# Optimization experiments

Measured on AMD Instinct MI355X. Metric: run time of the kernel, lower is better.

Reference implementation:

```python
import jax, jax.numpy as jnp
import numpy as np

EMBED = 1024
HEADS = 16
HEAD_DIM = EMBED // HEADS


def setup_inputs() -> dict:
    key = jax.random.key(0)
    ks = jax.random.split(key, 11)
    B, S, E = 4, 2048, EMBED
    scale = 1.0 / np.sqrt(E)
    inp = {
        "Q": jax.random.normal(ks[0], (B, S, E), jnp.float32),
        "K": jax.random.normal(ks[1], (B, S, E), jnp.float32),
        "V": jax.random.normal(ks[2], (B, S, E), jnp.float32),
        "Wq": jax.random.normal(ks[3], (E, E), jnp.float32) * scale,
        "Wk": jax.random.normal(ks[4], (E, E), jnp.float32) * scale,
        "Wv": jax.random.normal(ks[5], (E, E), jnp.float32) * scale,
        "Wo": jax.random.normal(ks[6], (E, E), jnp.float32) * scale,
        "bq": jax.random.normal(ks[7], (E,), jnp.float32) * 0.01,
        "bk": jax.random.normal(ks[8], (E,), jnp.float32) * 0.01,
        "bv": jax.random.normal(ks[9], (E,), jnp.float32) * 0.01,
        "bo": jax.random.normal(ks[10], (E,), jnp.float32) * 0.01,
    }
    return inp


def reference(Q, K, V, Wq, Wk, Wv, Wo, bq, bk, bv, bo):
    B, S, E = Q.shape
    H, Dh = HEADS, HEAD_DIM
    # linear projections (torch Linear: x @ W.T + b)
    q = (Q @ Wq.T + bq).reshape(B, S, H, Dh).transpose(0, 2, 1, 3)  # [B,H,S,Dh]
    k = (K @ Wk.T + bk).reshape(B, S, H, Dh).transpose(0, 2, 1, 3)
    v = (V @ Wv.T + bv).reshape(B, S, H, Dh).transpose(0, 2, 1, 3)
    # scores [B,H,S,S]
    A = jnp.einsum('bhqd,bhkd->bhqk', q, k) / np.sqrt(Dh).astype(np.float32)
    # causal mask (mask=True)
    causal = jnp.tril(jnp.ones((S, S), dtype=bool))
    A = jnp.where(causal, A, -jnp.inf)
    w = jax.nn.softmax(A, axis=-1)
    out = jnp.einsum('bhqk,bhkd->bhqd', w, v)  # [B,H,S,Dh]
    out = out.transpose(0, 2, 1, 3).reshape(B, S, E)
    return out @ Wo.T + bo
```

## Files before the change

### kernel.cpp

```cpp
#include <hip/hip_runtime.h>
#include <hip/hip_bf16.h>
#include <hip/hip_fp16.h>

#define E_DIM 1024
#define N_HEADS 16
#define DH 64
#define BATCH 4
#define SEQ 2048
#define MROWS (BATCH * SEQ)
#define NQT 16

using half8 = __attribute__((ext_vector_type(8))) _Float16;
using half4v = __attribute__((ext_vector_type(4))) _Float16;
using fp16x2 = __attribute__((ext_vector_type(2))) __fp16;
using f32x4 = __attribute__((ext_vector_type(4))) float;

#define LOG2E 1.44269504088896340736f

__device__ inline half8 ld8(const _Float16* p) { return *(const half8*)p; }

__device__ inline uint32_t lds_off(const void* p) {
    return (uint32_t)(uintptr_t)(const __attribute__((address_space(3))) char*)p;
}

__device__ inline float exp2fast(float x) {
    float r;
    asm("v_exp_f32 %0, %1" : "=v"(r) : "v"(x));
    return r;
}

__global__ void cast3_f16(const float* __restrict__ a0, const float* __restrict__ a1,
                          const float* __restrict__ a2,
                          _Float16* __restrict__ o0, _Float16* __restrict__ o1,
                          _Float16* __restrict__ o2, int n4) {
    const int z = blockIdx.y;
    const float* in = z == 0 ? a0 : z == 1 ? a1 : a2;
    _Float16* out = z == 0 ? o0 : z == 1 ? o1 : o2;
    int i = blockIdx.x * blockDim.x + threadIdx.x;
    if (i < n4) {
        float4 v = *(const float4*)(in + (size_t)i * 4);
        half4v o;
        o[0] = (_Float16)v.x; o[1] = (_Float16)v.y;
        o[2] = (_Float16)v.z; o[3] = (_Float16)v.w;
        *(half4v*)(out + (size_t)i * 4) = o;
    }
}
__global__ void cast4_f16(const float* __restrict__ a0, const float* __restrict__ a1,
                          const float* __restrict__ a2, const float* __restrict__ a3,
                          _Float16* __restrict__ o0, _Float16* __restrict__ o1,
                          _Float16* __restrict__ o2, _Float16* __restrict__ o3, int n4) {
    const int z = blockIdx.y;
    const float* in = z == 0 ? a0 : z == 1 ? a1 : z == 2 ? a2 : a3;
    _Float16* out = z == 0 ? o0 : z == 1 ? o1 : z == 2 ? o2 : o3;
    int i = blockIdx.x * blockDim.x + threadIdx.x;
    if (i < n4) {
        float4 v = *(const float4*)(in + (size_t)i * 4);
        half4v o;
        o[0] = (_Float16)v.x; o[1] = (_Float16)v.y;
        o[2] = (_Float16)v.z; o[3] = (_Float16)v.w;
        *(half4v*)(out + (size_t)i * 4) = o;
    }
}

template <int MODE>
__device__ __forceinline__ void gemm_body(
    const _Float16* __restrict__ A, const _Float16* __restrict__ Bt,
    const float* __restrict__ bias, void* __restrict__ outp,
    int N, int K, float scale, _Float16* As, _Float16* Bs)
{
    const int t = threadIdx.x;
    const int w = t >> 6, l = t & 63;
    const int wr = w >> 1, wc = w & 1;
    const int lr = l & 15, lg = l >> 4;
    const long row0 = (long)blockIdx.x * 128;
    const long col0 = (long)blockIdx.y * 128;
    f32x4 acc[4][4] = {};

    for (int k0 = 0; k0 < K; k0 += 32) {
        __syncthreads();
        #pragma unroll
        for (int p = 0; p < 2; ++p) {
            const int n = p * 256 + t;
            const int row = n >> 2, c8 = (n & 3) << 3;
            const _Float16* ga = &A[(size_t)(row0 + row) * K + k0 + c8];
            const _Float16* gb = &Bt[(size_t)(col0 + row) * K + k0 + c8];
            __builtin_amdgcn_global_load_lds(
                (const __attribute__((address_space(1))) unsigned int*)ga,
                (__attribute__((address_space(3))) unsigned int*)((char*)As + n * 16), 16, 0, 0);
            __builtin_amdgcn_global_load_lds(
                (const __attribute__((address_space(1))) unsigned int*)gb,
                (__attribute__((address_space(3))) unsigned int*)((char*)Bs + n * 16), 16, 0, 0);
        }
        __syncthreads();
        half8 af[4], bf[4];
        #pragma unroll
        for (int i = 0; i < 4; i++) {
            af[i] = *(const half8*)&As[(wr * 64 + i * 16 + lr) * 32 + lg * 8];
            bf[i] = *(const half8*)&Bs[(wc * 64 + i * 16 + lr) * 32 + lg * 8];
        }
        #pragma unroll
        for (int i = 0; i < 4; i++)
            #pragma unroll
            for (int j = 0; j < 4; j++)
                acc[i][j] = __builtin_amdgcn_mfma_f32_16x16x32_f16(af[i], bf[j], acc[i][j], 0, 0, 0);
    }

    #pragma unroll
    for (int i = 0; i < 4; i++)
        #pragma unroll
        for (int j = 0; j < 4; j++)
            #pragma unroll
            for (int r = 0; r < 4; r++) {
                long row = row0 + wr * 64 + i * 16 + lg * 4 + r;
                long col = col0 + wc * 64 + j * 16 + lr;
                float v = acc[i][j][r] + bias[col];
                if (MODE == 0) {
                    ((float*)outp)[row * N + col] = v;
                } else {
                    long b = row >> 11, s = row & 2047;
                    long h = col >> 6, d = col & 63;
                    ((_Float16*)outp)[(((b * N_HEADS + h) * SEQ + s) << 6) + d] =
                        (_Float16)(v * scale);
                }
            }
}

__global__ __launch_bounds__(256) void gemm_qkv(
    const _Float16* __restrict__ A0, const _Float16* __restrict__ A1,
    const _Float16* __restrict__ A2,
    const _Float16* __restrict__ W0, const _Float16* __restrict__ W1,
    const _Float16* __restrict__ W2,
    const float* __restrict__ b0, const float* __restrict__ b1,
    const float* __restrict__ b2,
    _Float16* __restrict__ o0, _Float16* __restrict__ o1, _Float16* __restrict__ o2)
{
    __shared__ _Float16 As[128 * 32];
    __shared__ _Float16 Bs[128 * 32];
    const int z = blockIdx.z;
    const _Float16* A = z == 0 ? A0 : z == 1 ? A1 : A2;
    const _Float16* W = z == 0 ? W0 : z == 1 ? W1 : W2;
    const float* bia = z == 0 ? b0 : z == 1 ? b1 : b2;
    _Float16* o = z == 0 ? o0 : z == 1 ? o1 : o2;
    const float scale = z == 0 ? (0.125f * LOG2E) : 1.0f;
    gemm_body<1>(A, W, bia, o, E_DIM, E_DIM, scale, As, Bs);
}

__global__ __launch_bounds__(256) void gemm_out(
    const _Float16* __restrict__ A, const _Float16* __restrict__ W,
    const float* __restrict__ bias, float* __restrict__ o)
{
    __shared__ _Float16 As[128 * 32];
    __shared__ _Float16 Bs[128 * 32];
    gemm_body<0>(A, W, bias, o, E_DIM, E_DIM, 1.0f, As, Bs);
}

__global__ __launch_bounds__(256) void attn_fwd(
    const _Float16* __restrict__ qb, const _Float16* __restrict__ kb,
    const _Float16* __restrict__ vb, _Float16* __restrict__ ob)
{
    __shared__ _Float16 sK[2 * 4096];
    __shared__ _Float16 sV[2 * 4096];
    const int bh = blockIdx.x;
    const int p = blockIdx.y;
    const int t = threadIdx.x;
    const int w = t >> 6, l = t & 63;
    const int lr = l & 15, lg = l >> 4;
    const _Float16* qh = qb + (size_t)bh * SEQ * DH;
    const _Float16* kh = kb + (size_t)bh * SEQ * DH;
    const _Float16* vh = vb + (size_t)bh * SEQ * DH;

    const int srow = t >> 3, sc16 = t & 7;
    const uint32_t kd0 = (uint32_t)((srow * 128 + sc16 * 16) ^ ((srow & 7) << 4));
    const uint32_t kd1 = (uint32_t)(((srow + 32) * 128 + sc16 * 16) ^ ((srow & 7) << 4));
    const uint32_t vd0 = (uint32_t)(((srow >> 2) * 256 + (sc16 >> 1) * 64 + (srow & 3) * 16 + (sc16 & 1) * 8) * 2);
    const uint32_t vd1 = (uint32_t)((((srow + 32) >> 2) * 256 + (sc16 >> 1) * 64 + (srow & 3) * 16 + (sc16 & 1) * 8) * 2);
    char* sKc = (char*)sK;
    char* sVc = (char*)sV;
    const uint32_t vldsbase = lds_off(sV);
    const int b = bh >> 4, h = bh & 15;

    #pragma unroll 1
    for (int seg = 0; seg < 2; ++seg) {
        const int tile = seg == 0 ? p : (NQT - 1 - p);
        const int nt = 2 * tile + 2;
        const int q0 = tile * 128 + w * 16;
        const int q1 = q0 + 64;

        half8 qf00 = ld8(&qh[(q0 + lr) * DH + lg * 8]);
        half8 qf01 = ld8(&qh[(q0 + lr) * DH + 32 + lg * 8]);
        half8 qf10 = ld8(&qh[(q1 + lr) * DH + lg * 8]);
        half8 qf11 = ld8(&qh[(q1 + lr) * DH + 32 + lg * 8]);

        f32x4 acc0[4] = {}, acc1[4] = {};
        float m0 = -1e30f, l0 = 0.f, m1 = -1e30f, l1 = 0.f;

        __syncthreads();
        {
            const _Float16* kp = &kh[srow * DH + sc16 * 8];
            const _Float16* vp = &vh[srow * DH + sc16 * 8];
            half8 a = ld8(kp), bb = ld8(kp + 32 * DH);
            half8 c = ld8(vp), d = ld8(vp + 32 * DH);
            *(half8*)(sKc + kd0) = a;
            *(half8*)(sKc + kd1) = bb;
            *(half8*)(sVc + vd0) = c;
            *(half8*)(sVc + vd1) = d;
        }
        __syncthreads();

        int cur = 0;
        for (int it = 0; it < nt; ++it) {
            half8 nk0, nk1, nv0, nv1;
            const bool more = (it + 1 < nt);
            if (more) {
                const _Float16* kp = &kh[((it + 1) * 64 + srow) * DH + sc16 * 8];
                const _Float16* vp = &vh[((it + 1) * 64 + srow) * DH + sc16 * 8];
                nk0 = ld8(kp); nk1 = ld8(kp + 32 * DH);
                nv0 = ld8(vp); nv1 = ld8(vp + 32 * DH);
            }

            const char* kbuf = sKc + (cur ? 8192 : 0);
            const uint32_t vbuf = vldsbase + (cur ? 8192u : 0u);
            const bool a0 = (it <= 2 * tile);
            const bool diag0 = (it == 2 * tile);
            const bool diag1 = (it == 2 * tile + 1);

            f32x4 st0[4], st1[4];
            __builtin_amdgcn_s_setprio(1);
            #pragma unroll
            for (int sub = 0; sub < 4; ++sub) {
                const int row = sub * 16 + lr;
                half8 kf0 = *(const half8*)(kbuf + ((row * 128 + lg * 16) ^ ((row & 7) << 4)));
                half8 kf1 = *(const half8*)(kbuf + ((row * 128 + 64 + lg * 16) ^ ((row & 7) << 4)));
                f32x4 s1 = {};
                s1 = __builtin_amdgcn_mfma_f32_16x16x32_f16(kf0, qf10, s1, 0, 0, 0);
                s1 = __builtin_amdgcn_mfma_f32_16x16x32_f16(kf1, qf11, s1, 0, 0, 0);
                st1[sub] = s1;
                if (a0) {
                    f32x4 s0 = {};
                    s0 = __builtin_amdgcn_mfma_f32_16x16x32_f16(kf0, qf00, s0, 0, 0, 0);
                    s0 = __builtin_amdgcn_mfma_f32_16x16x32_f16(kf1, qf01, s0, 0, 0, 0);
                    st0[sub] = s0;
                }
            }
            __builtin_amdgcn_s_setprio(0);

            half4v pa0[4], pa1[4];
            bool skip0 = true;
            if (a0) {
                if (diag0) {
                    #pragma unroll
                    for (int sub = 0; sub < 4; ++sub)
                        #pragma unroll
                        for (int r = 0; r < 4; ++r)
                            if (sub * 16 + lg * 4 + r > w * 16 + lr) st0[sub][r] = -1e30f;
                }
                float tmax = -1e30f;
                #pragma unroll
                for (int sub = 0; sub < 4; ++sub)
                    #pragma unroll
                    for (int r = 0; r < 4; ++r) tmax = fmaxf(tmax, st0[sub][r]);
                tmax = fmaxf(tmax, __shfl_xor(tmax, 16, 64));
                tmax = fmaxf(tmax, __shfl_xor(tmax, 32, 64));
                skip0 = __all(tmax <= m0 + 10.0f);
                float fscale = 1.0f;
                if (!skip0) {
                    const float m_new = fmaxf(m0, tmax);
                    fscale = exp2fast(m0 - m_new);
                    m0 = m_new;
                }
                float psum = 0.f;
                #pragma unroll
                for (int sub = 0; sub < 4; ++sub) {
                    float pv[4];
                    #pragma unroll
                    for (int r = 0; r < 4; ++r) { pv[r] = exp2fast(st0[sub][r] - m0); psum += pv[r]; }
                    fp16x2 lo = __builtin_amdgcn_cvt_pkrtz(pv[0], pv[1]);
                    fp16x2 hi = __builtin_amdgcn_cvt_pkrtz(pv[2], pv[3]);
                    pa0[sub][0] = (_Float16)lo[0]; pa0[sub][1] = (_Float16)lo[1];
                    pa0[sub][2] = (_Float16)hi[0]; pa0[sub][3] = (_Float16)hi[1];
                }
                l0 = l0 * fscale + psum;
                if (!skip0) {
                    #pragma unroll
                    for (int r = 0; r < 4; ++r) {
                        const float fr = __shfl(fscale, lg * 4 + r, 64);
                        acc0[0][r] *= fr; acc0[1][r] *= fr; acc0[2][r] *= fr; acc0[3][r] *= fr;
                    }
                }
            }

            {
                if (diag1) {
                    #pragma unroll
                    for (int sub = 0; sub < 4; ++sub)
                        #pragma unroll
                        for (int r = 0; r < 4; ++r)
                            if (sub * 16 + lg * 4 + r > w * 16 + lr) st1[sub][r] = -1e30f;
                }
                float tmax = -1e30f;
                #pragma unroll
                for (int sub = 0; sub < 4; ++sub)
                    #pragma unroll
                    for (int r = 0; r < 4; ++r) tmax = fmaxf(tmax, st1[sub][r]);
                tmax = fmaxf(tmax, __shfl_xor(tmax, 16, 64));
                tmax = fmaxf(tmax, __shfl_xor(tmax, 32, 64));
                const bool skip = __all(tmax <= m1 + 10.0f);
                float fscale = 1.0f;
                if (!skip) {
                    const float m_new = fmaxf(m1, tmax);
                    fscale = exp2fast(m1 - m_new);
                    m1 = m_new;
                }
                float psum = 0.f;
                #pragma unroll
                for (int sub = 0; sub < 4; ++sub) {
                    float pv[4];
                    #pragma unroll
                    for (int r = 0; r < 4; ++r) { pv[r] = exp2fast(st1[sub][r] - m1); psum += pv[r]; }
                    fp16x2 lo = __builtin_amdgcn_cvt_pkrtz(pv[0], pv[1]);
                    fp16x2 hi = __builtin_amdgcn_cvt_pkrtz(pv[2], pv[3]);
                    pa1[sub][0] = (_Float16)lo[0]; pa1[sub][1] = (_Float16)lo[1];
                    pa1[sub][2] = (_Float16)hi[0]; pa1[sub][3] = (_Float16)hi[1];
                }
                l1 = l1 * fscale + psum;
                if (!skip) {
                    #pragma unroll
                    for (int r = 0; r < 4; ++r) {
                        const float fr = __shfl(fscale, lg * 4 + r, 64);
                        acc1[0][r] *= fr; acc1[1][r] *= fr; acc1[2][r] *= fr; acc1[3][r] *= fr;
                    }
                }
            }

            __builtin_amdgcn_s_setprio(1);
            #pragma unroll
            for (int sub = 0; sub < 4; ++sub) {
                const uint32_t a0addr = vbuf + (uint32_t)((sub * 4 + lg) * 512 + lr * 8);
                half4v vf0, vf1, vf2, vf3;
                asm volatile("ds_read_b64_tr_b16 %0, %1" : "=v"(vf0) : "v"(a0addr));
                asm volatile("ds_read_b64_tr_b16 %0, %1 offset:128" : "=v"(vf1) : "v"(a0addr));
                asm volatile("ds_read_b64_tr_b16 %0, %1 offset:256" : "=v"(vf2) : "v"(a0addr));
                asm volatile("ds_read_b64_tr_b16 %0, %1 offset:384" : "=v"(vf3) : "v"(a0addr));
                asm volatile("s_waitcnt lgkmcnt(0)");
                __builtin_amdgcn_sched_barrier(0);
                acc1[0] = __builtin_amdgcn_mfma_f32_16x16x16f16(pa1[sub], vf0, acc1[0], 0, 0, 0);
                acc1[1] = __builtin_amdgcn_mfma_f32_16x16x16f16(pa1[sub], vf1, acc1[1], 0, 0, 0);
                acc1[2] = __builtin_amdgcn_mfma_f32_16x16x16f16(pa1[sub], vf2, acc1[2], 0, 0, 0);
                acc1[3] = __builtin_amdgcn_mfma_f32_16x16x16f16(pa1[sub], vf3, acc1[3], 0, 0, 0);
                if (a0) {
                    acc0[0] = __builtin_amdgcn_mfma_f32_16x16x16f16(pa0[sub], vf0, acc0[0], 0, 0, 0);
                    acc0[1] = __builtin_amdgcn_mfma_f32_16x16x16f16(pa0[sub], vf1, acc0[1], 0, 0, 0);
                    acc0[2] = __builtin_amdgcn_mfma_f32_16x16x16f16(pa0[sub], vf2, acc0[2], 0, 0, 0);
                    acc0[3] = __builtin_amdgcn_mfma_f32_16x16x16f16(pa0[sub], vf3, acc0[3], 0, 0, 0);
                }
            }
            __builtin_amdgcn_s_setprio(0);

            if (more) {
                char* kd = sKc + (cur ? 0 : 8192);
                char* vd = sVc + (cur ? 0 : 8192);
                *(half8*)(kd + kd0) = nk0;
                *(half8*)(kd + kd1) = nk1;
                *(half8*)(vd + vd0) = nv0;
                *(half8*)(vd + vd1) = nv1;
            }
            __syncthreads();
            cur ^= 1;
        }

        l0 += __shfl_xor(l0, 16, 64); l0 += __shfl_xor(l0, 32, 64);
        l1 += __shfl_xor(l1, 16, 64); l1 += __shfl_xor(l1, 32, 64);
        const float inv0 = 1.f / l0, inv1 = 1.f / l1;
        #pragma unroll
        for (int r = 0; r < 4; ++r) {
            const float ir0 = __shfl(inv0, lg * 4 + r, 64);
            const float ir1 = __shfl(inv1, lg * 4 + r, 64);
            const int qr0 = q0 + lg * 4 + r;
            const int qr1 = q1 + lg * 4 + r;
            #pragma unroll
            for (int db = 0; db < 4; ++db) {
                ob[((size_t)(b * SEQ + qr0)) * E_DIM + h * DH + db * 16 + lr] =
                    (_Float16)(acc0[db][r] * ir0);
                ob[((size_t)(b * SEQ + qr1)) * E_DIM + h * DH + db * 16 + lr] =
                    (_Float16)(acc1[db][r] * ir1);
            }
        }
    }
}

extern "C" void kernel_launch(void* const* d_in, const int* in_sizes, int n_in,
                              void* d_out, int out_size, void* d_ws, size_t ws_size,
                              hipStream_t stream) {
    const float* Q  = (const float*)d_in[0];
    const float* K  = (const float*)d_in[1];
    const float* V  = (const float*)d_in[2];
    const float* Wq = (const float*)d_in[3];
    const float* Wk = (const float*)d_in[4];
    const float* Wv = (const float*)d_in[5];
    const float* Wo = (const float*)d_in[6];
    const float* bq = (const float*)d_in[7];
    const float* bk = (const float*)d_in[8];
    const float* bv = (const float*)d_in[9];
    const float* bo = (const float*)d_in[10];

    const size_t NX = (size_t)MROWS * E_DIM;
    const size_t NW = (size_t)E_DIM * E_DIM;

    _Float16* ws  = (_Float16*)d_ws;
    _Float16* Xq  = ws;
    _Float16* Xk  = Xq + NX;
    _Float16* Xv  = Xk + NX;
    _Float16* hWq = Xv + NX;
    _Float16* hWk = hWq + NW;
    _Float16* hWv = hWk + NW;
    _Float16* hWo = hWv + NW;
    _Float16* qbf = hWo + NW;
    _Float16* kbf = qbf + NX;
    _Float16* vbf = kbf + NX;
    _Float16* aof = vbf + NX;

    const int n4x = (int)(NX / 4), n4w = (int)(NW / 4);
    cast3_f16<<<dim3((n4x + 255) / 256, 3), 256, 0, stream>>>(Q, K, V, Xq, Xk, Xv, n4x);
    cast4_f16<<<dim3((n4w + 255) / 256, 4), 256, 0, stream>>>(Wq, Wk, Wv, Wo, hWq, hWk, hWv, hWo, n4w);

    dim3 gg3(MROWS / 128, E_DIM / 128, 3);
    gemm_qkv<<<gg3, 256, 0, stream>>>(Xq, Xk, Xv, hWq, hWk, hWv, bq, bk, bv, qbf, kbf, vbf);

    attn_fwd<<<dim3(BATCH * N_HEADS, NQT / 2), 256, 0, stream>>>(qbf, kbf, vbf, aof);

    dim3 gg(MROWS / 128, E_DIM / 128);
    gemm_out<<<gg, 256, 0, stream>>>(aof, hWo, bo, (float*)d_out);
}
```

Before: 219.1 us.

## Stream K/V tiles into triple-buffered LDS via direct global-to-LDS loads

Replaces the register-staged double-buffered K/V loads in the attention kernel with direct global_load_lds transfers into a three-slot LDS ring, prefetching two tiles ahead with vmcnt waits and one barrier per iteration. The swizzle moves from the LDS write address to the global read address, so the existing read layout is kept. The change also uses a tree-shaped max reduction and fdot2-based row sums on the packed fp16 probabilities. It uses more LDS (48KB), which may lower occupancy, and the row sums are now taken from the fp16-rounded values.

```diff
diff --git a/kernel.cpp b/kernel.cpp
--- a/kernel.cpp
+++ b/kernel.cpp
@@ -158,26 +158,29 @@
     const _Float16* __restrict__ qb, const _Float16* __restrict__ kb,
     const _Float16* __restrict__ vb, _Float16* __restrict__ ob)
 {
-    __shared__ _Float16 sK[2 * 4096];
-    __shared__ _Float16 sV[2 * 4096];
+    __shared__ _Float16 sB[3 * 8192];
     const int bh = blockIdx.x;
     const int p = blockIdx.y;
     const int t = threadIdx.x;
     const int w = t >> 6, l = t & 63;
     const int lr = l & 15, lg = l >> 4;
     const _Float16* qh = qb + (size_t)bh * SEQ * DH;
-    const _Float16* kh = kb + (size_t)bh * SEQ * DH;
-    const _Float16* vh = vb + (size_t)bh * SEQ * DH;
-
-    const int srow = t >> 3, sc16 = t & 7;
-    const uint32_t kd0 = (uint32_t)((srow * 128 + sc16 * 16) ^ ((srow & 7) << 4));
-    const uint32_t kd1 = (uint32_t)(((srow + 32) * 128 + sc16 * 16) ^ ((srow & 7) << 4));
-    const uint32_t vd0 = (uint32_t)(((srow >> 2) * 256 + (sc16 >> 1) * 64 + (srow & 3) * 16 + (sc16 & 1) * 8) * 2);
-    const uint32_t vd1 = (uint32_t)((((srow + 32) >> 2) * 256 + (sc16 >> 1) * 64 + (srow & 3) * 16 + (sc16 & 1) * 8) * 2);
-    char* sKc = (char*)sK;
-    char* sVc = (char*)sV;
-    const uint32_t vldsbase = lds_off(sV);
+    const char* khc = (const char*)(kb + (size_t)bh * SEQ * DH);
+    const char* vhc = (const char*)(vb + (size_t)bh * SEQ * DH);
+    char* sBc = (char*)sB;
+    const uint32_t ldsbase = lds_off(sB);
     const int b = bh >> 4, h = bh & 15;
+
+    int koff[2], voff[2];
+    #pragma unroll
+    for (int i = 0; i < 2; ++i) {
+        const int s = i * 256 + t;
+        { const int r = s >> 3, c = (s & 7) ^ (r & 7);
+          koff[i] = r * 128 + c * 16; }
+        { const int r = ((s >> 5) << 2) | ((s >> 1) & 3);
+          const int c = (((s >> 3) & 3) << 1) | (s & 1);
+          voff[i] = r * 128 + c * 16; }
+    }
 
     #pragma unroll 1
     for (int seg = 0; seg < 2; ++seg) {
@@ -186,40 +189,48 @@
         const int q0 = tile * 128 + w * 16;
         const int q1 = q0 + 64;
 
+        __syncthreads();
+
         half8 qf00 = ld8(&qh[(q0 + lr) * DH + lg * 8]);
         half8 qf01 = ld8(&qh[(q0 + lr) * DH + 32 + lg * 8]);
         half8 qf10 = ld8(&qh[(q1 + lr) * DH + lg * 8]);
         half8 qf11 = ld8(&qh[(q1 + lr) * DH + 32 + lg * 8]);
 
+        #define STAGE(TI, BUF) do {                                                   \
+            const char* ks_ = khc + (size_t)(TI) * 8192;                              \
+            const char* vs_ = vhc + (size_t)(TI) * 8192;                              \
+            char* kd_ = sBc + (BUF) * 16384;                                          \
+            char* vd_ = kd_ + 8192;                                                   \
+            _Pragma("unroll")                                                         \
+            for (int i_ = 0; i_ < 2; ++i_) {                                          \
+                __builtin_amdgcn_global_load_lds(                                     \
+                    (const __attribute__((address_space(1))) unsigned int*)(ks_ + koff[i_]), \
+                    (__attribute__((address_space(3))) unsigned int*)(kd_ + i_ * 4096 + t * 16), 16, 0, 0); \
+                __builtin_amdgcn_global_load_lds(                                     \
+                    (const __attribute__((address_space(1))) unsigned int*)(vs_ + voff[i_]), \
+                    (__attribute__((address_space(3))) unsigned int*)(vd_ + i_ * 4096 + t * 16), 16, 0, 0); \
+            }                                                                         \
+        } while (0)
+
+        STAGE(0, 0);
+        STAGE(1, 1);
+
         f32x4 acc0[4] = {}, acc1[4] = {};
         float m0 = -1e30f, l0 = 0.f, m1 = -1e30f, l1 = 0.f;
 
-        __syncthreads();
-        {
-            const _Float16* kp = &kh[srow * DH + sc16 * 8];
-            const _Float16* vp = &vh[srow * DH + sc16 * 8];
-            half8 a = ld8(kp), bb = ld8(kp + 32 * DH);
-            half8 c = ld8(vp), d = ld8(vp + 32 * DH);
-            *(half8*)(sKc + kd0) = a;
-            *(half8*)(sKc + kd1) = bb;
-            *(half8*)(sVc + vd0) = c;
-            *(half8*)(sVc + vd1) = d;
-        }
-        __syncthreads();
-
         int cur = 0;
+        #pragma unroll 1
         for (int it = 0; it < nt; ++it) {
-            half8 nk0, nk1, nv0, nv1;
-            const bool more = (it + 1 < nt);
-            if (more) {
-                const _Float16* kp = &kh[((it + 1) * 64 + srow) * DH + sc16 * 8];
-                const _Float16* vp = &vh[((it + 1) * 64 + srow) * DH + sc16 * 8];
-                nk0 = ld8(kp); nk1 = ld8(kp + 32 * DH);
-                nv0 = ld8(vp); nv1 = ld8(vp + 32 * DH);
-            }
-
-            const char* kbuf = sKc + (cur ? 8192 : 0);
-            const uint32_t vbuf = vldsbase + (cur ? 8192u : 0u);
+            if (it + 1 < nt) asm volatile("s_waitcnt vmcnt(4)" ::: "memory");
+            else             asm volatile("s_waitcnt vmcnt(0)" ::: "memory");
+            __builtin_amdgcn_s_barrier();
+            if (it + 2 < nt) {
+                int nb = cur + 2; if (nb >= 3) nb -= 3;
+                STAGE(it + 2, nb);
+            }
+
+            const char* kbuf = sBc + cur * 16384;
+            const uint32_t vbuf = ldsbase + (uint32_t)cur * 16384u + 8192u;
             const bool a0 = (it <= 2 * tile);
             const bool diag0 = (it == 2 * tile);
             const bool diag1 = (it == 2 * tile + 1);
@@ -245,7 +256,7 @@
             __builtin_amdgcn_s_setprio(0);
 
             half4v pa0[4], pa1[4];
-            bool skip0 = true;
+
             if (a0) {
                 if (diag0) {
                     #pragma unroll
@@ -254,33 +265,33 @@
                         for (int r = 0; r < 4; ++r)
                             if (sub * 16 + lg * 4 + r > w * 16 + lr) st0[sub][r] = -1e30f;
                 }
-                float tmax = -1e30f;
-                #pragma unroll
-                for (int sub = 0; sub < 4; ++sub)
-                    #pragma unroll
-                    for (int r = 0; r < 4; ++r) tmax = fmaxf(tmax, st0[sub][r]);
+                float a = fmaxf(fmaxf(st0[0][0], st0[0][1]), st0[0][2]);
+                float bb = fmaxf(fmaxf(st0[0][3], st0[1][0]), st0[1][1]);
+                float c = fmaxf(fmaxf(st0[1][2], st0[1][3]), st0[2][0]);
+                float d = fmaxf(fmaxf(st0[2][1], st0[2][2]), st0[2][3]);
+                float e = fmaxf(fmaxf(st0[3][0], st0[3][1]), st0[3][2]);
+                float tmax = fmaxf(fmaxf(fmaxf(a, bb), fmaxf(c, d)), fmaxf(e, st0[3][3]));
                 tmax = fmaxf(tmax, __shfl_xor(tmax, 16, 64));
                 tmax = fmaxf(tmax, __shfl_xor(tmax, 32, 64));
-                skip0 = __all(tmax <= m0 + 10.0f);
+                const bool skip = __all(tmax <= m0 + 10.0f);
                 float fscale = 1.0f;
-                if (!skip0) {
-                    const float m_new = fmaxf(m0, tmax);
-                    fscale = exp2fast(m0 - m_new);
-                    m0 = m_new;
-                }
+                if (!skip) { const float mn = fmaxf(m0, tmax); fscale = exp2fast(m0 - mn); m0 = mn; }
                 float psum = 0.f;
+                fp16x2 ones; ones[0] = (__fp16)1.f; ones[1] = (__fp16)1.f;
                 #pragma unroll
                 for (int sub = 0; sub < 4; ++sub) {
                     float pv[4];
                     #pragma unroll
-                    for (int r = 0; r < 4; ++r) { pv[r] = exp2fast(st0[sub][r] - m0); psum += pv[r]; }
+                    for (int r = 0; r < 4; ++r) pv[r] = exp2fast(st0[sub][r] - m0);
                     fp16x2 lo = __builtin_amdgcn_cvt_pkrtz(pv[0], pv[1]);
                     fp16x2 hi = __builtin_amdgcn_cvt_pkrtz(pv[2], pv[3]);
+                    psum = __builtin_amdgcn_fdot2(lo, ones, psum, false);
+                    psum = __builtin_amdgcn_fdot2(hi, ones, psum, false);
                     pa0[sub][0] = (_Float16)lo[0]; pa0[sub][1] = (_Float16)lo[1];
                     pa0[sub][2] = (_Float16)hi[0]; pa0[sub][3] = (_Float16)hi[1];
                 }
                 l0 = l0 * fscale + psum;
-                if (!skip0) {
+                if (!skip) {
                     #pragma unroll
                     for (int r = 0; r < 4; ++r) {
                         const float fr = __shfl(fscale, lg * 4 + r, 64);
@@ -297,28 +308,28 @@
                         for (int r = 0; r < 4; ++r)
                             if (sub * 16 + lg * 4 + r > w * 16 + lr) st1[sub][r] = -1e30f;
                 }
-                float tmax = -1e30f;
-                #pragma unroll
-                for (int sub = 0; sub < 4; ++sub)
-                    #pragma unroll
-                    for (int r = 0; r < 4; ++r) tmax = fmaxf(tmax, st1[sub][r]);
+                float a = fmaxf(fmaxf(st1[0][0], st1[0][1]), st1[0][2]);
+                float bb = fmaxf(fmaxf(st1[0][3], st1[1][0]), st1[1][1]);
+                float c = fmaxf(fmaxf(st1[1][2], st1[1][3]), st1[2][0]);
+                float d = fmaxf(fmaxf(st1[2][1], st1[2][2]), st1[2][3]);
+                float e = fmaxf(fmaxf(st1[3][0], st1[3][1]), st1[3][2]);
+                float tmax = fmaxf(fmaxf(fmaxf(a, bb), fmaxf(c, d)), fmaxf(e, st1[3][3]));
                 tmax = fmaxf(tmax, __shfl_xor(tmax, 16, 64));
                 tmax = fmaxf(tmax, __shfl_xor(tmax, 32, 64));
                 const bool skip = __all(tmax <= m1 + 10.0f);
                 float fscale = 1.0f;
-                if (!skip) {
-                    const float m_new = fmaxf(m1, tmax);
-                    fscale = exp2fast(m1 - m_new);
-                    m1 = m_new;
-                }
+                if (!skip) { const float mn = fmaxf(m1, tmax); fscale = exp2fast(m1 - mn); m1 = mn; }
                 float psum = 0.f;
+                fp16x2 ones; ones[0] = (__fp16)1.f; ones[1] = (__fp16)1.f;
                 #pragma unroll
                 for (int sub = 0; sub < 4; ++sub) {
                     float pv[4];
                     #pragma unroll
-                    for (int r = 0; r < 4; ++r) { pv[r] = exp2fast(st1[sub][r] - m1); psum += pv[r]; }
+                    for (int r = 0; r < 4; ++r) pv[r] = exp2fast(st1[sub][r] - m1);
                     fp16x2 lo = __builtin_amdgcn_cvt_pkrtz(pv[0], pv[1]);
                     fp16x2 hi = __builtin_amdgcn_cvt_pkrtz(pv[2], pv[3]);
+                    psum = __builtin_amdgcn_fdot2(lo, ones, psum, false);
+                    psum = __builtin_amdgcn_fdot2(hi, ones, psum, false);
                     pa1[sub][0] = (_Float16)lo[0]; pa1[sub][1] = (_Float16)lo[1];
                     pa1[sub][2] = (_Float16)hi[0]; pa1[sub][3] = (_Float16)hi[1];
                 }
@@ -356,16 +367,7 @@
             }
             __builtin_amdgcn_s_setprio(0);
 
-            if (more) {
-                char* kd = sKc + (cur ? 0 : 8192);
-                char* vd = sVc + (cur ? 0 : 8192);
-                *(half8*)(kd + kd0) = nk0;
-                *(half8*)(kd + kd1) = nk1;
-                *(half8*)(vd + vd0) = nv0;
-                *(half8*)(vd + vd1) = nv1;
-            }
-            __syncthreads();
-            cur ^= 1;
+            cur = (cur + 1 == 3) ? 0 : cur + 1;
         }
 
         l0 += __shfl_xor(l0, 16, 64); l0 += __shfl_xor(l0, 32, 64);
@@ -385,6 +387,7 @@
                     (_Float16)(acc1[db][r] * ir1);
             }
         }
+        #undef STAGE
     }
 }
 
```

Measured after the change: 201.1 us. 8.2% less time.
